# Performance work log

Hardware: AMD Instinct MI355X
Metric: run time of the kernel (lower is better)

The kernel has to match this reference:

```python
import jax, jax.numpy as jnp
import numpy as np


def setup_inputs() -> dict:
    key = jax.random.key(0)
    k1, k2, k3 = jax.random.split(key, 3)
    B, N, D = 4096, 8192, 1024
    protein_features = jax.random.normal(k1, (B, D), dtype=jnp.float32)
    function_features = jax.random.normal(k2, (N, D), dtype=jnp.float32)
    positive_mask = jax.random.randint(k3, (B, N), 0, 2, dtype=jnp.int32)
    temperature = jnp.zeros((1,), dtype=jnp.float32)  # exp(0) = 1
    return {
        "protein_features": protein_features,
        "function_features": function_features,
        "positive_mask": positive_mask,
        "temperature": temperature,
    }


def reference(protein_features, function_features, positive_mask, temperature):
    # logits: [B, N]
    logits = jnp.matmul(protein_features, function_features.T) / jnp.exp(temperature[0])
    # row-wise logsumexp, computed ONCE per row (the torch loop recomputes it per positive)
    lse = jax.nn.logsumexp(logits, axis=1, keepdims=True)  # [B, 1]
    m = (positive_mask == 1).astype(logits.dtype)          # [B, N]
    n_pos = m.sum()
    # per-pair loss = -pos_logit + logsumexp(row); mean over all positive pairs
    loss_sum = ((lse - logits) * m).sum()
    return jnp.where(n_pos > 0, loss_sum / n_pos, jnp.zeros((), dtype=logits.dtype))
```

## Files before the change

### kernel.cpp

```cpp
#include <hip/hip_runtime.h>
#include <hip/hip_bf16.h>

typedef __attribute__((ext_vector_type(4))) float f32x4;
typedef __attribute__((ext_vector_type(8))) __bf16 bf16x8;
typedef __attribute__((ext_vector_type(8))) unsigned short u16x8;

constexpr int BROWS = 4096;
constexpr int NCOLS = 8192;
constexpr int DK    = 1024;
constexpr int BM = 256, BN = 256, BK = 64;
constexpr int NCB = NCOLS / BN;
constexpr int NKT = DK / BK;
constexpr int NIT = NKT / 2;
constexpr int NWRDS = BROWS * NCOLS / 64;

__device__ static inline unsigned short f2bf(float f) {
  unsigned int u = __builtin_bit_cast(unsigned int, f);
  u += 0x7FFFu + ((u >> 16) & 1u);
  return (unsigned short)(u >> 16);
}

__device__ static inline void gload16(const void* g, void* l) {
  __builtin_amdgcn_global_load_lds(
      (const __attribute__((address_space(1))) void*)g,
      (__attribute__((address_space(3))) void*)l, 16, 0, 0);
}

__global__ void convert_kernel(const float* __restrict__ src,
                               unsigned short* __restrict__ dst,
                               int n4, int applyScale,
                               const float* __restrict__ temp) {
  float scale = applyScale ? expf(-temp[0]) : 1.0f;
  int i = blockIdx.x * blockDim.x + threadIdx.x;
  if (i >= n4) return;
  float4 v = reinterpret_cast<const float4*>(src)[i];
  ushort4 o;
  o.x = f2bf(v.x * scale);
  o.y = f2bf(v.y * scale);
  o.z = f2bf(v.z * scale);
  o.w = f2bf(v.w * scale);
  reinterpret_cast<ushort4*>(dst)[i] = o;
}

__global__ void maskpack_kernel(const int* __restrict__ mask,
                                unsigned long long* __restrict__ bits) {
  const int lane = threadIdx.x & 63;
  const int gw   = (blockIdx.x * blockDim.x + threadIdx.x) >> 6;
  const int nw   = (gridDim.x * blockDim.x) >> 6;
  for (int base = gw * 8; base < NWRDS; base += nw * 8) {
    int v[8];
#pragma unroll
    for (int j = 0; j < 8; ++j)
      v[j] = mask[(size_t)(base + j) * 64 + lane];
#pragma unroll
    for (int j = 0; j < 8; ++j) {
      unsigned long long bm = __ballot(v[j] == 1);
      if (lane == 0) bits[base + j] = bm;
    }
  }
}

__device__ __forceinline__ void stage_half(const unsigned short* __restrict__ g,
                                           unsigned short* l, int t, int kt) {
#pragma unroll
  for (int p = 0; p < 2; ++p) {
    const int off = p * 8192 + t * 16;
    const int row = off >> 7;
    const int keSw = ((off & 127) >> 1) ^ ((row & 7) << 3);
    gload16(g + (size_t)row * DK + kt * 64 + keSw, l + (off >> 1));
  }
}

#define MFMA_BF16 __builtin_amdgcn_mfma_f32_16x16x32_bf16

#define LDS_FRAG(base, row, kk)                                             \
  __builtin_bit_cast(bf16x8, *reinterpret_cast<const u16x8*>(               \
      &(base)[((row) * 64 + (kk) * 32 + l4 * 8) ^ (((row) & 7) << 3)]))

#define READ_A(b, q)                                              \
  aFr[0][0] = LDS_FRAG(As[b][wm], (2*(q)    )*16 + l15, 0);       \
  aFr[0][1] = LDS_FRAG(As[b][wm], (2*(q)    )*16 + l15, 1);       \
  aFr[1][0] = LDS_FRAG(As[b][wm], (2*(q) + 1)*16 + l15, 0);       \
  aFr[1][1] = LDS_FRAG(As[b][wm], (2*(q) + 1)*16 + l15, 1);

#define READ_B(b)                                                 \
  bFr[0][0] = LDS_FRAG(Bs[b][bhB], brB +  0 + l15, 0);            \
  bFr[0][1] = LDS_FRAG(Bs[b][bhB], brB +  0 + l15, 1);            \
  bFr[1][0] = LDS_FRAG(Bs[b][bhB], brB + 16 + l15, 0);            \
  bFr[1][1] = LDS_FRAG(Bs[b][bhB], brB + 16 + l15, 1);            \
  bFr[2][0] = LDS_FRAG(Bs[b][bhB], brB + 32 + l15, 0);            \
  bFr[2][1] = LDS_FRAG(Bs[b][bhB], brB + 32 + l15, 1);            \
  bFr[3][0] = LDS_FRAG(Bs[b][bhB], brB + 48 + l15, 0);            \
  bFr[3][1] = LDS_FRAG(Bs[b][bhB], brB + 48 + l15, 1);

#define COMPUTE(q)                                                                  \
  __builtin_amdgcn_s_setprio(1);                                                   \
  _Pragma("unroll") for (int mm = 0; mm < 2; ++mm)                                  \
  _Pragma("unroll") for (int n = 0; n < 4; ++n) {                                   \
    acc[2*(q)+mm][n] = MFMA_BF16(aFr[mm][0], bFr[n][0], acc[2*(q)+mm][n], 0, 0, 0); \
    acc[2*(q)+mm][n] = MFMA_BF16(aFr[mm][1], bFr[n][1], acc[2*(q)+mm][n], 0, 0, 0); \
  }                                                                                 \
  __builtin_amdgcn_s_setprio(0);

#define PHASE_MID                                    \
  __builtin_amdgcn_s_barrier();                      \
  asm volatile("s_waitcnt lgkmcnt(0)" ::: "memory");

#define PHASE_END                                    \
  __builtin_amdgcn_s_barrier();

__global__ __launch_bounds__(512, 2)
void main_kernel(const unsigned short* __restrict__ Pb,
                 const unsigned short* __restrict__ Fb,
                 const unsigned long long* __restrict__ bits,
                 f32x4* __restrict__ partials) {
  __shared__ __align__(16) unsigned short As[2][2][128 * 64];
  __shared__ __align__(16) unsigned short Bs[2][2][128 * 64];
  __shared__ float redM[4][256], redS[4][256], redP[4][256], redC[4][256];

  const int t    = threadIdx.x;
  const int lane = t & 63;
  const int w    = t >> 6;
  const int wm   = w >> 2;
  const int wn   = w & 3;
  const int l15  = lane & 15;
  const int l4   = lane >> 4;
  const int bhB  = wn >> 1;
  const int brB  = (wn & 1) * 64;

  const int brow = blockIdx.y * BM;
  const int bcol = blockIdx.x * BN;

  const unsigned short* Ag0 = Pb + (size_t)brow * DK;
  const unsigned short* Ag1 = Pb + (size_t)(brow + 128) * DK;
  const unsigned short* Bg0 = Fb + (size_t)bcol * DK;
  const unsigned short* Bg1 = Fb + (size_t)(bcol + 128) * DK;

  f32x4 acc[8][4] = {};
  bf16x8 bFr[4][2];
  bf16x8 aFr[2][2];

  stage_half(Bg0, Bs[0][0], t, 0);
  stage_half(Bg1, Bs[0][1], t, 0);
  stage_half(Ag0, As[0][0], t, 0);
  stage_half(Ag1, As[0][1], t, 0);
  stage_half(Bg0, Bs[1][0], t, 1);
  stage_half(Bg1, Bs[1][1], t, 1);
  asm volatile("s_waitcnt vmcnt(4)" ::: "memory");
  __builtin_amdgcn_s_barrier();

  for (int i = 0; i < NIT; ++i) {
    const int t1 = 2 * i + 1;
    const bool more = (i < NIT - 1);
    READ_B(0); READ_A(0, 0);
    stage_half(Ag0, As[1][0], t, t1);
    PHASE_MID; COMPUTE(0); PHASE_END;
    READ_A(0, 1);
    stage_half(Ag1, As[1][1], t, t1);
    PHASE_MID; COMPUTE(1); PHASE_END;
    READ_A(0, 2);
    if (more) stage_half(Bg0, Bs[0][0], t, t1 + 1);
    PHASE_MID; COMPUTE(2); PHASE_END;
    READ_A(0, 3);
    if (more) stage_half(Bg1, Bs[0][1], t, t1 + 1);
    PHASE_MID; COMPUTE(3);
    if (more) { asm volatile("s_waitcnt vmcnt(4)" ::: "memory"); }
    else      { asm volatile("s_waitcnt vmcnt(0)" ::: "memory"); }
    PHASE_END;
    READ_B(1); READ_A(1, 0);
    if (more) stage_half(Ag0, As[0][0], t, t1 + 1);
    PHASE_MID; COMPUTE(0); PHASE_END;
    READ_A(1, 1);
    if (more) stage_half(Ag1, As[0][1], t, t1 + 1);
    PHASE_MID; COMPUTE(1); PHASE_END;
    READ_A(1, 2);
    if (more) stage_half(Bg0, Bs[1][0], t, t1 + 2);
    PHASE_MID; COMPUTE(2); PHASE_END;
    READ_A(1, 3);
    if (more) stage_half(Bg1, Bs[1][1], t, t1 + 2);
    PHASE_MID; COMPUTE(3);
    if (more) { asm volatile("s_waitcnt vmcnt(4)" ::: "memory"); }
    PHASE_END;
  }

#pragma unroll
  for (int m = 0; m < 8; ++m) {
#pragma unroll
    for (int r = 0; r < 4; ++r) {
      float v0 = acc[m][0][r], v1 = acc[m][1][r], v2 = acc[m][2][r], v3 = acc[m][3][r];
      float mx = fmaxf(fmaxf(v0, v1), fmaxf(v2, v3));
#pragma unroll
      for (int s = 1; s < 16; s <<= 1) mx = fmaxf(mx, __shfl_xor(mx, s, 64));
      float se = __expf(v0 - mx) + __expf(v1 - mx) + __expf(v2 - mx) + __expf(v3 - mx);

      const int lr = wm * 128 + m * 16 + l4 * 4 + r;
      const unsigned long long wB =
          bits[(size_t)(brow + lr) * (NCOLS / 64) + (bcol >> 6) + wn];
      float ps = 0.f, pc = 0.f;
      if ((wB >> (l15     )) & 1ull) { ps += v0; pc += 1.f; }
      if ((wB >> (l15 + 16)) & 1ull) { ps += v1; pc += 1.f; }
      if ((wB >> (l15 + 32)) & 1ull) { ps += v2; pc += 1.f; }
      if ((wB >> (l15 + 48)) & 1ull) { ps += v3; pc += 1.f; }
#pragma unroll
      for (int s = 1; s < 16; s <<= 1) {
        se += __shfl_xor(se, s, 64);
        ps += __shfl_xor(ps, s, 64);
        pc += __shfl_xor(pc, s, 64);
      }
      if (l15 == 0) {
        redM[wn][lr] = mx;
        redS[wn][lr] = se;
        redP[wn][lr] = ps;
        redC[wn][lr] = pc;
      }
    }
  }
  __syncthreads();

  if (t < 256) {
    float m0 = redM[0][t], m1 = redM[1][t], m2 = redM[2][t], m3 = redM[3][t];
    float m  = fmaxf(fmaxf(m0, m1), fmaxf(m2, m3));
    float s  = redS[0][t] * __expf(m0 - m) + redS[1][t] * __expf(m1 - m)
             + redS[2][t] * __expf(m2 - m) + redS[3][t] * __expf(m3 - m);
    float ps = redP[0][t] + redP[1][t] + redP[2][t] + redP[3][t];
    float pc = redC[0][t] + redC[1][t] + redC[2][t] + redC[3][t];
    f32x4 out4;
    out4.x = m; out4.y = s; out4.z = ps; out4.w = pc;
    partials[(size_t)(brow + t) * NCB + blockIdx.x] = out4;
  }
}

__global__ void row_reduce_kernel(const f32x4* __restrict__ partials,
                                  float* __restrict__ rowContrib,
                                  float* __restrict__ rowCnt) {
  const int row  = blockIdx.x * 4 + (threadIdx.x >> 6);
  const int lane = threadIdx.x & 63;
  f32x4 p = partials[(size_t)row * NCB + (lane & 31)];
  float m = p.x;
#pragma unroll
  for (int s = 1; s < 32; s <<= 1) m = fmaxf(m, __shfl_xor(m, s, 64));
  float se = p.y * __expf(p.x - m);
  float ps = p.z, pc = p.w;
#pragma unroll
  for (int s = 1; s < 32; s <<= 1) {
    se += __shfl_xor(se, s, 64);
    ps += __shfl_xor(ps, s, 64);
    pc += __shfl_xor(pc, s, 64);
  }
  if (lane == 0) {
    float lse = m + logf(se);
    rowContrib[row] = pc * lse - ps;
    rowCnt[row]     = pc;
  }
}

__global__ void final_kernel(const float* __restrict__ rowContrib,
                             const float* __restrict__ rowCnt,
                             float* __restrict__ out) {
  __shared__ double sC[256];
  __shared__ double sN[256];
  double c = 0.0, n = 0.0;
  for (int i = threadIdx.x; i < BROWS; i += 256) {
    c += (double)rowContrib[i];
    n += (double)rowCnt[i];
  }
  sC[threadIdx.x] = c;
  sN[threadIdx.x] = n;
  __syncthreads();
  for (int s = 128; s > 0; s >>= 1) {
    if ((int)threadIdx.x < s) {
      sC[threadIdx.x] += sC[threadIdx.x + s];
      sN[threadIdx.x] += sN[threadIdx.x + s];
    }
    __syncthreads();
  }
  if (threadIdx.x == 0) out[0] = (sN[0] > 0.0) ? (float)(sC[0] / sN[0]) : 0.0f;
}

extern "C" void kernel_launch(void* const* d_in, const int* in_sizes, int n_in,
                              void* d_out, int out_size, void* d_ws, size_t ws_size,
                              hipStream_t stream) {
  const float* P    = (const float*)d_in[0];
  const float* F    = (const float*)d_in[1];
  const int*   mask = (const int*)d_in[2];
  const float* temp = (const float*)d_in[3];
  float* out = (float*)d_out;

  char* ws = (char*)d_ws;
  unsigned short* Pb = (unsigned short*)ws;
  unsigned short* Fb = (unsigned short*)(ws + (size_t)BROWS * DK * 2);
  unsigned long long* bits = (unsigned long long*)(ws + (size_t)(BROWS + NCOLS) * DK * 2);
  f32x4* partials    = (f32x4*)((char*)bits + (size_t)NWRDS * 8);
  float* rowContrib  = (float*)((char*)partials + (size_t)BROWS * NCB * sizeof(f32x4));
  float* rowCnt      = rowContrib + BROWS;

  const int nP4 = BROWS * DK / 4;
  const int nF4 = NCOLS * DK / 4;
  hipLaunchKernelGGL(convert_kernel, dim3(nP4 / 256), dim3(256), 0, stream, P, Pb, nP4, 1, temp);
  hipLaunchKernelGGL(convert_kernel, dim3(nF4 / 256), dim3(256), 0, stream, F, Fb, nF4, 0, temp);
  hipLaunchKernelGGL(maskpack_kernel, dim3(2048), dim3(256), 0, stream, mask, bits);
  hipLaunchKernelGGL(main_kernel, dim3(NCOLS / BN, BROWS / BM), dim3(512), 0, stream, Pb, Fb, bits, partials);
  hipLaunchKernelGGL(row_reduce_kernel, dim3(BROWS / 4), dim3(256), 0, stream, partials, rowContrib, rowCnt);
  hipLaunchKernelGGL(final_kernel, dim3(1), dim3(256), 0, stream, rowContrib, rowCnt, out);
}
```

Before: 139.7 us.

## Vectorize mask packing with interleaved bit layout and halve main loop phases

The mask pack kernel now reads int4 per lane and emits four ballots per load, which produces an interleaved bit layout. The epilogue's bit indexing is changed to match that layout. The GEMM main loop is restructured from four phases per K tile to two larger phases, reading four A fragments and issuing 32 MFMAs between barriers. This halves the barrier count but raises register pressure and coarsens the overlap between loads and compute.

Measured after the change: 137.7 us. About the same (-1.4%).

```diff
diff --git a/kernel.cpp b/kernel.cpp
--- a/kernel.cpp
+++ b/kernel.cpp
@@ -47,15 +47,22 @@
   const int lane = threadIdx.x & 63;
   const int gw   = (blockIdx.x * blockDim.x + threadIdx.x) >> 6;
   const int nw   = (gridDim.x * blockDim.x) >> 6;
-  for (int base = gw * 8; base < NWRDS; base += nw * 8) {
-    int v[8];
+  constexpr int NG = BROWS * NCOLS / 256;
+  for (int base = gw * 8; base < NG; base += nw * 8) {
+    int4 v[8];
 #pragma unroll
     for (int j = 0; j < 8; ++j)
-      v[j] = mask[(size_t)(base + j) * 64 + lane];
+      v[j] = reinterpret_cast<const int4*>(mask)[(size_t)(base + j) * 64 + lane];
 #pragma unroll
     for (int j = 0; j < 8; ++j) {
-      unsigned long long bm = __ballot(v[j] == 1);
-      if (lane == 0) bits[base + j] = bm;
+      unsigned long long b0 = __ballot(v[j].x == 1);
+      unsigned long long b1 = __ballot(v[j].y == 1);
+      unsigned long long b2 = __ballot(v[j].z == 1);
+      unsigned long long b3 = __ballot(v[j].w == 1);
+      if (lane == 0) {
+        ulonglong4 o; o.x = b0; o.y = b1; o.z = b2; o.w = b3;
+        reinterpret_cast<ulonglong4*>(bits)[base + j] = o;
+      }
     }
   }
 }
@@ -77,11 +84,15 @@
   __builtin_bit_cast(bf16x8, *reinterpret_cast<const u16x8*>(               \
       &(base)[((row) * 64 + (kk) * 32 + l4 * 8) ^ (((row) & 7) << 3)]))
 
-#define READ_A(b, q)                                              \
-  aFr[0][0] = LDS_FRAG(As[b][wm], (2*(q)    )*16 + l15, 0);       \
-  aFr[0][1] = LDS_FRAG(As[b][wm], (2*(q)    )*16 + l15, 1);       \
-  aFr[1][0] = LDS_FRAG(As[b][wm], (2*(q) + 1)*16 + l15, 0);       \
-  aFr[1][1] = LDS_FRAG(As[b][wm], (2*(q) + 1)*16 + l15, 1);
+#define READ_A4(b, h)                                                   \
+  aFr[0][0] = LDS_FRAG(As[b][wm], ((h)*4+0)*16 + l15, 0);               \
+  aFr[0][1] = LDS_FRAG(As[b][wm], ((h)*4+0)*16 + l15, 1);               \
+  aFr[1][0] = LDS_FRAG(As[b][wm], ((h)*4+1)*16 + l15, 0);               \
+  aFr[1][1] = LDS_FRAG(As[b][wm], ((h)*4+1)*16 + l15, 1);               \
+  aFr[2][0] = LDS_FRAG(As[b][wm], ((h)*4+2)*16 + l15, 0);               \
+  aFr[2][1] = LDS_FRAG(As[b][wm], ((h)*4+2)*16 + l15, 1);               \
+  aFr[3][0] = LDS_FRAG(As[b][wm], ((h)*4+3)*16 + l15, 0);               \
+  aFr[3][1] = LDS_FRAG(As[b][wm], ((h)*4+3)*16 + l15, 1);
 
 #define READ_B(b)                                                 \
   bFr[0][0] = LDS_FRAG(Bs[b][bhB], brB +  0 + l15, 0);            \
@@ -93,13 +104,13 @@
   bFr[3][0] = LDS_FRAG(Bs[b][bhB], brB + 48 + l15, 0);            \
   bFr[3][1] = LDS_FRAG(Bs[b][bhB], brB + 48 + l15, 1);
 
-#define COMPUTE(q)                                                                  \
-  __builtin_amdgcn_s_setprio(1);                                                   \
-  _Pragma("unroll") for (int mm = 0; mm < 2; ++mm)                                  \
-  _Pragma("unroll") for (int n = 0; n < 4; ++n) {                                   \
-    acc[2*(q)+mm][n] = MFMA_BF16(aFr[mm][0], bFr[n][0], acc[2*(q)+mm][n], 0, 0, 0); \
-    acc[2*(q)+mm][n] = MFMA_BF16(aFr[mm][1], bFr[n][1], acc[2*(q)+mm][n], 0, 0, 0); \
-  }                                                                                 \
+#define COMPUTE32(h)                                                                  \
+  __builtin_amdgcn_s_setprio(1);                                                     \
+  _Pragma("unroll") for (int mm = 0; mm < 4; ++mm)                                    \
+  _Pragma("unroll") for (int n = 0; n < 4; ++n) {                                     \
+    acc[(h)*4+mm][n] = MFMA_BF16(aFr[mm][0], bFr[n][0], acc[(h)*4+mm][n], 0, 0, 0);   \
+    acc[(h)*4+mm][n] = MFMA_BF16(aFr[mm][1], bFr[n][1], acc[(h)*4+mm][n], 0, 0, 0);   \
+  }                                                                                   \
   __builtin_amdgcn_s_setprio(0);
 
 #define PHASE_MID                                    \
@@ -138,7 +149,7 @@
 
   f32x4 acc[8][4] = {};
   bf16x8 bFr[4][2];
-  bf16x8 aFr[2][2];
+  bf16x8 aFr[4][2];
 
   stage_half(Bg0, Bs[0][0], t, 0);
   stage_half(Bg1, Bs[0][1], t, 0);
@@ -150,35 +161,33 @@
   __builtin_amdgcn_s_barrier();
 
   for (int i = 0; i < NIT; ++i) {
-    const int t1 = 2 * i + 1;
+    const int t0 = 2 * i, t1 = 2 * i + 1;
     const bool more = (i < NIT - 1);
-    READ_B(0); READ_A(0, 0);
+    READ_B(0); READ_A4(0, 0);
     stage_half(Ag0, As[1][0], t, t1);
-    PHASE_MID; COMPUTE(0); PHASE_END;
-    READ_A(0, 1);
     stage_half(Ag1, As[1][1], t, t1);
-    PHASE_MID; COMPUTE(1); PHASE_END;
-    READ_A(0, 2);
-    if (more) stage_half(Bg0, Bs[0][0], t, t1 + 1);
-    PHASE_MID; COMPUTE(2); PHASE_END;
-    READ_A(0, 3);
-    if (more) stage_half(Bg1, Bs[0][1], t, t1 + 1);
-    PHASE_MID; COMPUTE(3);
+    PHASE_MID; COMPUTE32(0); PHASE_END;
+    READ_A4(0, 1);
+    if (more) {
+      stage_half(Bg0, Bs[0][0], t, t0 + 2);
+      stage_half(Bg1, Bs[0][1], t, t0 + 2);
+    }
+    PHASE_MID; COMPUTE32(1);
     if (more) { asm volatile("s_waitcnt vmcnt(4)" ::: "memory"); }
     else      { asm volatile("s_waitcnt vmcnt(0)" ::: "memory"); }
     PHASE_END;
-    READ_B(1); READ_A(1, 0);
-    if (more) stage_half(Ag0, As[0][0], t, t1 + 1);
-    PHASE_MID; COMPUTE(0); PHASE_END;
-    READ_A(1, 1);
-    if (more) stage_half(Ag1, As[0][1], t, t1 + 1);
-    PHASE_MID; COMPUTE(1); PHASE_END;
-    READ_A(1, 2);
-    if (more) stage_half(Bg0, Bs[1][0], t, t1 + 2);
-    PHASE_MID; COMPUTE(2); PHASE_END;
-    READ_A(1, 3);
-    if (more) stage_half(Bg1, Bs[1][1], t, t1 + 2);
-    PHASE_MID; COMPUTE(3);
+    READ_B(1); READ_A4(1, 0);
+    if (more) {
+      stage_half(Ag0, As[0][0], t, t0 + 2);
+      stage_half(Ag1, As[0][1], t, t0 + 2);
+    }
+    PHASE_MID; COMPUTE32(0); PHASE_END;
+    READ_A4(1, 1);
+    if (more) {
+      stage_half(Bg0, Bs[1][0], t, t1 + 2);
+      stage_half(Bg1, Bs[1][1], t, t1 + 2);
+    }
+    PHASE_MID; COMPUTE32(1);
     if (more) { asm volatile("s_waitcnt vmcnt(4)" ::: "memory"); }
     PHASE_END;
   }
@@ -195,12 +204,13 @@
 
       const int lr = wm * 128 + m * 16 + l4 * 4 + r;
       const unsigned long long wB =
-          bits[(size_t)(brow + lr) * (NCOLS / 64) + (bcol >> 6) + wn];
+          bits[(size_t)(brow + lr) * (NCOLS / 64) + (size_t)blockIdx.x * 4 + (l15 & 3)];
+      const int bsh = wn * 16 + (l15 >> 2);
       float ps = 0.f, pc = 0.f;
-      if ((wB >> (l15     )) & 1ull) { ps += v0; pc += 1.f; }
-      if ((wB >> (l15 + 16)) & 1ull) { ps += v1; pc += 1.f; }
-      if ((wB >> (l15 + 32)) & 1ull) { ps += v2; pc += 1.f; }
-      if ((wB >> (l15 + 48)) & 1ull) { ps += v3; pc += 1.f; }
+      if ((wB >> (bsh     )) & 1ull) { ps += v0; pc += 1.f; }
+      if ((wB >> (bsh +  4)) & 1ull) { ps += v1; pc += 1.f; }
+      if ((wB >> (bsh +  8)) & 1ull) { ps += v2; pc += 1.f; }
+      if ((wB >> (bsh + 12)) & 1ull) { ps += v3; pc += 1.f; }
 #pragma unroll
       for (int s = 1; s < 16; s <<= 1) {
         se += __shfl_xor(se, s, 64);
```

## Switch GEMM to FP8 e4m3 scaled MFMA and vectorize mask bit-packing

Applied to the files above, without the earlier changes.

Inputs are now quantized to FP8 e4m3 instead of bf16, and the main GEMM uses the 16x16x128 f8f6f4 scaled MFMA with a doubled K tile and 128-byte LDS rows. This halves operand traffic and the number of MFMA issues, at the cost of much lower input precision in the logits. The mask packer now loads int4 vectors and emits four ballots per lane, which changes the bit layout, so the epilogue's bit indexing is adjusted to match. The FP8 logits may drift enough from the reference to break tolerance.

Result: slower. 406.4 us (+190.9%).

```diff
diff --git a/kernel.cpp b/kernel.cpp
--- a/kernel.cpp
+++ b/kernel.cpp
@@ -1,45 +1,45 @@
 #include <hip/hip_runtime.h>
 #include <hip/hip_bf16.h>
+#include <hip/hip_fp8.h>
 
 typedef __attribute__((ext_vector_type(4))) float f32x4;
-typedef __attribute__((ext_vector_type(8))) __bf16 bf16x8;
-typedef __attribute__((ext_vector_type(8))) unsigned short u16x8;
+typedef __attribute__((ext_vector_type(4))) int   i32x4;
+typedef __attribute__((ext_vector_type(8))) int   i32x8;
 
 constexpr int BROWS = 4096;
 constexpr int NCOLS = 8192;
 constexpr int DK    = 1024;
-constexpr int BM = 256, BN = 256, BK = 64;
+constexpr int BM = 256, BN = 256, BK = 128;
 constexpr int NCB = NCOLS / BN;
 constexpr int NKT = DK / BK;
 constexpr int NIT = NKT / 2;
 constexpr int NWRDS = BROWS * NCOLS / 64;
 
-__device__ static inline unsigned short f2bf(float f) {
-  unsigned int u = __builtin_bit_cast(unsigned int, f);
-  u += 0x7FFFu + ((u >> 16) & 1u);
-  return (unsigned short)(u >> 16);
-}
-
 __device__ static inline void gload16(const void* g, void* l) {
   __builtin_amdgcn_global_load_lds(
       (const __attribute__((address_space(1))) void*)g,
       (__attribute__((address_space(3))) void*)l, 16, 0, 0);
 }
 
-__global__ void convert_kernel(const float* __restrict__ src,
-                               unsigned short* __restrict__ dst,
-                               int n4, int applyScale,
-                               const float* __restrict__ temp) {
+__global__ void convert8_kernel(const float* __restrict__ src,
+                                unsigned char* __restrict__ dst,
+                                int n8, int applyScale,
+                                const float* __restrict__ temp) {
   float scale = applyScale ? expf(-temp[0]) : 1.0f;
   int i = blockIdx.x * blockDim.x + threadIdx.x;
-  if (i >= n4) return;
-  float4 v = reinterpret_cast<const float4*>(src)[i];
-  ushort4 o;
-  o.x = f2bf(v.x * scale);
-  o.y = f2bf(v.y * scale);
-  o.z = f2bf(v.z * scale);
-  o.w = f2bf(v.w * scale);
-  reinterpret_cast<ushort4*>(dst)[i] = o;
+  if (i >= n8) return;
+  const float4* s = reinterpret_cast<const float4*>(src) + (size_t)i * 2;
+  float4 v0 = s[0], v1 = s[1];
+  union { unsigned char b[8]; uint2 u; } o;
+  o.b[0] = __hip_fp8_e4m3(v0.x * scale).__x;
+  o.b[1] = __hip_fp8_e4m3(v0.y * scale).__x;
+  o.b[2] = __hip_fp8_e4m3(v0.z * scale).__x;
+  o.b[3] = __hip_fp8_e4m3(v0.w * scale).__x;
+  o.b[4] = __hip_fp8_e4m3(v1.x * scale).__x;
+  o.b[5] = __hip_fp8_e4m3(v1.y * scale).__x;
+  o.b[6] = __hip_fp8_e4m3(v1.z * scale).__x;
+  o.b[7] = __hip_fp8_e4m3(v1.w * scale).__x;
+  reinterpret_cast<uint2*>(dst)[i] = o.u;
 }
 
 __global__ void maskpack_kernel(const int* __restrict__ mask,
@@ -47,59 +47,73 @@
   const int lane = threadIdx.x & 63;
   const int gw   = (blockIdx.x * blockDim.x + threadIdx.x) >> 6;
   const int nw   = (gridDim.x * blockDim.x) >> 6;
-  for (int base = gw * 8; base < NWRDS; base += nw * 8) {
-    int v[8];
+  constexpr int NG = BROWS * NCOLS / 256;
+  for (int base = gw * 8; base < NG; base += nw * 8) {
+    int4 v[8];
 #pragma unroll
     for (int j = 0; j < 8; ++j)
-      v[j] = mask[(size_t)(base + j) * 64 + lane];
+      v[j] = reinterpret_cast<const int4*>(mask)[(size_t)(base + j) * 64 + lane];
 #pragma unroll
     for (int j = 0; j < 8; ++j) {
-      unsigned long long bm = __ballot(v[j] == 1);
-      if (lane == 0) bits[base + j] = bm;
+      unsigned long long b0 = __ballot(v[j].x == 1);
+      unsigned long long b1 = __ballot(v[j].y == 1);
+      unsigned long long b2 = __ballot(v[j].z == 1);
+      unsigned long long b3 = __ballot(v[j].w == 1);
+      if (lane == 0) {
+        ulonglong4 o; o.x = b0; o.y = b1; o.z = b2; o.w = b3;
+        reinterpret_cast<ulonglong4*>(bits)[base + j] = o;
+      }
     }
   }
 }
 
-__device__ __forceinline__ void stage_half(const unsigned short* __restrict__ g,
-                                           unsigned short* l, int t, int kt) {
+__device__ __forceinline__ void stage_half(const unsigned char* __restrict__ g,
+                                           unsigned char* l, int t, int kt) {
 #pragma unroll
   for (int p = 0; p < 2; ++p) {
     const int off = p * 8192 + t * 16;
     const int row = off >> 7;
-    const int keSw = ((off & 127) >> 1) ^ ((row & 7) << 3);
-    gload16(g + (size_t)row * DK + kt * 64 + keSw, l + (off >> 1));
-  }
-}
-
-#define MFMA_BF16 __builtin_amdgcn_mfma_f32_16x16x32_bf16
-
-#define LDS_FRAG(base, row, kk)                                             \
-  __builtin_bit_cast(bf16x8, *reinterpret_cast<const u16x8*>(               \
-      &(base)[((row) * 64 + (kk) * 32 + l4 * 8) ^ (((row) & 7) << 3)]))
-
-#define READ_A(b, q)                                              \
-  aFr[0][0] = LDS_FRAG(As[b][wm], (2*(q)    )*16 + l15, 0);       \
-  aFr[0][1] = LDS_FRAG(As[b][wm], (2*(q)    )*16 + l15, 1);       \
-  aFr[1][0] = LDS_FRAG(As[b][wm], (2*(q) + 1)*16 + l15, 0);       \
-  aFr[1][1] = LDS_FRAG(As[b][wm], (2*(q) + 1)*16 + l15, 1);
-
-#define READ_B(b)                                                 \
-  bFr[0][0] = LDS_FRAG(Bs[b][bhB], brB +  0 + l15, 0);            \
-  bFr[0][1] = LDS_FRAG(Bs[b][bhB], brB +  0 + l15, 1);            \
-  bFr[1][0] = LDS_FRAG(Bs[b][bhB], brB + 16 + l15, 0);            \
-  bFr[1][1] = LDS_FRAG(Bs[b][bhB], brB + 16 + l15, 1);            \
-  bFr[2][0] = LDS_FRAG(Bs[b][bhB], brB + 32 + l15, 0);            \
-  bFr[2][1] = LDS_FRAG(Bs[b][bhB], brB + 32 + l15, 1);            \
-  bFr[3][0] = LDS_FRAG(Bs[b][bhB], brB + 48 + l15, 0);            \
-  bFr[3][1] = LDS_FRAG(Bs[b][bhB], brB + 48 + l15, 1);
-
-#define COMPUTE(q)                                                                  \
-  __builtin_amdgcn_s_setprio(1);                                                   \
-  _Pragma("unroll") for (int mm = 0; mm < 2; ++mm)                                  \
-  _Pragma("unroll") for (int n = 0; n < 4; ++n) {                                   \
-    acc[2*(q)+mm][n] = MFMA_BF16(aFr[mm][0], bFr[n][0], acc[2*(q)+mm][n], 0, 0, 0); \
-    acc[2*(q)+mm][n] = MFMA_BF16(aFr[mm][1], bFr[n][1], acc[2*(q)+mm][n], 0, 0, 0); \
-  }                                                                                 \
+    const int colSw = (off & 127) ^ ((row & 7) << 4);
+    gload16(g + (size_t)row * DK + kt * 128 + colSw, l + off);
+  }
+}
+
+#define LDS_F4(base, row, h)                                                \
+  (*reinterpret_cast<const i32x4*>(                                         \
+      &(base)[(((row) * 128 + l4 * 32 + (h) * 16) ^ (((row) & 7) << 4))]))
+
+__device__ __forceinline__ i32x8 cat8(i32x4 lo, i32x4 hi) {
+  i32x8 r;
+  r[0] = lo[0]; r[1] = lo[1]; r[2] = lo[2]; r[3] = lo[3];
+  r[4] = hi[0]; r[5] = hi[1]; r[6] = hi[2]; r[7] = hi[3];
+  return r;
+}
+
+#define MFMA_FP8(a, b, c) \
+  __builtin_amdgcn_mfma_scale_f32_16x16x128_f8f6f4((a), (b), (c), 0, 0, 0, 127, 0, 127)
+
+#define READ_A(b, q)                                                          \
+  aF[0] = cat8(LDS_F4(As[b][wm], (2*(q)    )*16 + l15, 0),                    \
+               LDS_F4(As[b][wm], (2*(q)    )*16 + l15, 1));                   \
+  aF[1] = cat8(LDS_F4(As[b][wm], (2*(q) + 1)*16 + l15, 0),                    \
+               LDS_F4(As[b][wm], (2*(q) + 1)*16 + l15, 1));
+
+#define READ_B(b)                                                             \
+  bF[0] = cat8(LDS_F4(Bs[b][bhB], brB +  0 + l15, 0),                         \
+               LDS_F4(Bs[b][bhB], brB +  0 + l15, 1));                        \
+  bF[1] = cat8(LDS_F4(Bs[b][bhB], brB + 16 + l15, 0),                         \
+               LDS_F4(Bs[b][bhB], brB + 16 + l15, 1));                        \
+  bF[2] = cat8(LDS_F4(Bs[b][bhB], brB + 32 + l15, 0),                         \
+               LDS_F4(Bs[b][bhB], brB + 32 + l15, 1));                        \
+  bF[3] = cat8(LDS_F4(Bs[b][bhB], brB + 48 + l15, 0),                         \
+               LDS_F4(Bs[b][bhB], brB + 48 + l15, 1));
+
+#define COMPUTE(q)                                                            \
+  __builtin_amdgcn_s_setprio(1);                                             \
+  _Pragma("unroll") for (int mm = 0; mm < 2; ++mm)                            \
+  _Pragma("unroll") for (int n = 0; n < 4; ++n) {                             \
+    acc[2*(q)+mm][n] = MFMA_FP8(aF[mm], bF[n], acc[2*(q)+mm][n]);             \
+  }                                                                           \
   __builtin_amdgcn_s_setprio(0);
 
 #define PHASE_MID                                    \
@@ -110,12 +124,12 @@
   __builtin_amdgcn_s_barrier();
 
 __global__ __launch_bounds__(512, 2)
-void main_kernel(const unsigned short* __restrict__ Pb,
-                 const unsigned short* __restrict__ Fb,
+void main_kernel(const unsigned char* __restrict__ Pb,
+                 const unsigned char* __restrict__ Fb,
                  const unsigned long long* __restrict__ bits,
                  f32x4* __restrict__ partials) {
-  __shared__ __align__(16) unsigned short As[2][2][128 * 64];
-  __shared__ __align__(16) unsigned short Bs[2][2][128 * 64];
+  __shared__ __align__(16) unsigned char As[2][2][128 * 128];
+  __shared__ __align__(16) unsigned char Bs[2][2][128 * 128];
   __shared__ float redM[4][256], redS[4][256], redP[4][256], redC[4][256];
 
   const int t    = threadIdx.x;
@@ -131,14 +145,14 @@
   const int brow = blockIdx.y * BM;
   const int bcol = blockIdx.x * BN;
 
-  const unsigned short* Ag0 = Pb + (size_t)brow * DK;
-  const unsigned short* Ag1 = Pb + (size_t)(brow + 128) * DK;
-  const unsigned short* Bg0 = Fb + (size_t)bcol * DK;
-  const unsigned short* Bg1 = Fb + (size_t)(bcol + 128) * DK;
+  const unsigned char* Ag0 = Pb + (size_t)brow * DK;
+  const unsigned char* Ag1 = Pb + (size_t)(brow + 128) * DK;
+  const unsigned char* Bg0 = Fb + (size_t)bcol * DK;
+  const unsigned char* Bg1 = Fb + (size_t)(bcol + 128) * DK;
 
   f32x4 acc[8][4] = {};
-  bf16x8 bFr[4][2];
-  bf16x8 aFr[2][2];
+  i32x8 bF[4];
+  i32x8 aF[2];
 
   stage_half(Bg0, Bs[0][0], t, 0);
   stage_half(Bg1, Bs[0][1], t, 0);
@@ -195,12 +209,13 @@
 
       const int lr = wm * 128 + m * 16 + l4 * 4 + r;
       const unsigned long long wB =
-          bits[(size_t)(brow + lr) * (NCOLS / 64) + (bcol >> 6) + wn];
+          bits[(size_t)(brow + lr) * (NCOLS / 64) + (size_t)blockIdx.x * 4 + (l15 & 3)];
+      const int bsh = wn * 16 + (l15 >> 2);
       float ps = 0.f, pc = 0.f;
-      if ((wB >> (l15     )) & 1ull) { ps += v0; pc += 1.f; }
-      if ((wB >> (l15 + 16)) & 1ull) { ps += v1; pc += 1.f; }
-      if ((wB >> (l15 + 32)) & 1ull) { ps += v2; pc += 1.f; }
-      if ((wB >> (l15 + 48)) & 1ull) { ps += v3; pc += 1.f; }
+      if ((wB >> (bsh     )) & 1ull) { ps += v0; pc += 1.f; }
+      if ((wB >> (bsh +  4)) & 1ull) { ps += v1; pc += 1.f; }
+      if ((wB >> (bsh +  8)) & 1ull) { ps += v2; pc += 1.f; }
+      if ((wB >> (bsh + 12)) & 1ull) { ps += v3; pc += 1.f; }
 #pragma unroll
       for (int s = 1; s < 16; s <<= 1) {
         se += __shfl_xor(se, s, 64);
@@ -287,19 +302,19 @@
   float* out = (float*)d_out;
 
   char* ws = (char*)d_ws;
-  unsigned short* Pb = (unsigned short*)ws;
-  unsigned short* Fb = (unsigned short*)(ws + (size_t)BROWS * DK * 2);
-  unsigned long long* bits = (unsigned long long*)(ws + (size_t)(BROWS + NCOLS) * DK * 2);
+  unsigned char* Pb8 = (unsigned char*)ws;
+  unsigned char* Fb8 = (unsigned char*)(ws + (size_t)BROWS * DK);
+  unsigned long long* bits = (unsigned long long*)(ws + (size_t)(BROWS + NCOLS) * DK);
   f32x4* partials    = (f32x4*)((char*)bits + (size_t)NWRDS * 8);
   float* rowContrib  = (float*)((char*)partials + (size_t)BROWS * NCB * sizeof(f32x4));
   float* rowCnt      = rowContrib + BROWS;
 
-  const int nP4 = BROWS * DK / 4;
-  const int nF4 = NCOLS * DK / 4;
-  hipLaunchKernelGGL(convert_kernel, dim3(nP4 / 256), dim3(256), 0, stream, P, Pb, nP4, 1, temp);
-  hipLaunchKernelGGL(convert_kernel, dim3(nF4 / 256), dim3(256), 0, stream, F, Fb, nF4, 0, temp);
+  const int nP8 = BROWS * DK / 8;
+  const int nF8 = NCOLS * DK / 8;
+  hipLaunchKernelGGL(convert8_kernel, dim3(nP8 / 256), dim3(256), 0, stream, P, Pb8, nP8, 1, temp);
+  hipLaunchKernelGGL(convert8_kernel, dim3(nF8 / 256), dim3(256), 0, stream, F, Fb8, nF8, 0, temp);
   hipLaunchKernelGGL(maskpack_kernel, dim3(2048), dim3(256), 0, stream, mask, bits);
-  hipLaunchKernelGGL(main_kernel, dim3(NCOLS / BN, BROWS / BM), dim3(512), 0, stream, Pb, Fb, bits, partials);
+  hipLaunchKernelGGL(main_kernel, dim3(NCOLS / BN, BROWS / BM), dim3(512), 0, stream, Pb8, Fb8, bits, partials);
   hipLaunchKernelGGL(row_reduce_kernel, dim3(BROWS / 4), dim3(256), 0, stream, partials, rowContrib, rowCnt);
   hipLaunchKernelGGL(final_kernel, dim3(1), dim3(256), 0, stream, rowContrib, rowCnt, out);
 }
```
